# Performance work log

Measured on AMD Instinct MI355X. Metric: run time of the kernel, lower is better.

The kernel has to match this reference:

```python
import jax, jax.numpy as jnp
import numpy as np

S, B, C = 7, 2, 80
LAMBDA_COORDS = 5.0
LAMBDA_NOOBJ = 0.5


def _iou_cxcywh(a, b):
    """Elementwise IoU of boxes in cx,cy,w,h format, shapes (..., 4) -> (...).
    Same math as torchvision box_convert(cxcywh->xyxy) + box_iou diagonal,
    computed directly (O(S^2)) instead of the O(S^4) pairwise matrix."""
    ax1 = a[..., 0] - a[..., 2] * 0.5
    ay1 = a[..., 1] - a[..., 3] * 0.5
    ax2 = a[..., 0] + a[..., 2] * 0.5
    ay2 = a[..., 1] + a[..., 3] * 0.5
    bx1 = b[..., 0] - b[..., 2] * 0.5
    by1 = b[..., 1] - b[..., 3] * 0.5
    bx2 = b[..., 0] + b[..., 2] * 0.5
    by2 = b[..., 1] + b[..., 3] * 0.5
    inter_w = jnp.clip(jnp.minimum(ax2, bx2) - jnp.maximum(ax1, bx1), 0.0)
    inter_h = jnp.clip(jnp.minimum(ay2, by2) - jnp.maximum(ay1, by1), 0.0)
    inter = inter_w * inter_h
    area_a = (ax2 - ax1) * (ay2 - ay1)
    area_b = (bx2 - bx1) * (by2 - by1)
    return inter / (area_a + area_b - inter)


def setup_inputs() -> dict:
    key = jax.random.key(0)
    k1, k2 = jax.random.split(key)
    N = 8192
    predictions = jax.random.normal(k1, (N, S, S, C + 5 * B), dtype=jnp.float32)
    target = jax.random.uniform(k2, (N, S, S, C + 5), dtype=jnp.float32)
    return {"predictions": predictions, "target": target}


def reference(predictions, target):
    preds = predictions.reshape(-1, S, S, C + 5 * B)
    target_boxes = target[..., -4:]                 # (N,S,S,4)
    pred_boxes_1 = preds[..., -4:]
    pred_boxes_2 = preds[..., -9:-5]

    iou1 = _iou_cxcywh(pred_boxes_1, target_boxes)  # (N,S,S) == diag of box_iou
    iou2 = _iou_cxcywh(pred_boxes_2, target_boxes)
    ious_idx = jnp.argmax(jnp.stack([iou1, iou2], axis=0), axis=0)  # (N,S,S)

    m1 = (1 - ious_idx).astype(preds.dtype)  # responsible-box masks
    m2 = ious_idx.astype(preds.dtype)
    obj = target[..., -5]                    # objectness (N,S,S)

    pred_boxes = obj[..., None] * (m1[..., None] * pred_boxes_1 + m2[..., None] * pred_boxes_2)

    dims = jnp.sign(pred_boxes[..., -2:]) * jnp.sqrt(jnp.abs(pred_boxes[..., -2:]) + 1e-6)
    target_dims = jnp.sqrt(target_boxes[..., -2:])

    sse = lambda a, b: jnp.sum((a - b) ** 2)  # MSELoss(reduction='sum')

    center_loss = sse(pred_boxes[..., :-3], target_boxes[..., :-3]) * LAMBDA_COORDS
    dimensions_loss = sse(dims, target_dims) * LAMBDA_COORDS
    coords_loss = center_loss + dimensions_loss

    obj_pred = preds[..., -5] * m1 + preds[..., -10] * m2
    obj_loss = sse(obj * obj_pred, obj)
    noobj_loss = sse((1.0 - obj) * obj_pred, obj) * LAMBDA_NOOBJ

    classes_loss = sse(preds[..., :-10] * obj[..., None], target[..., :-5])

    return (coords_loss, obj_loss, noobj_loss, classes_loss)
```

## Files before the change

### kernel.cpp

```cpp
#include <hip/hip_runtime.h>
#include <stdint.h>


#define NPRED 90
#define NTGT  85
#define NCLS  80
#define CHUNK 32
#define TPB   256
#define NBLK  768

#define NT4 (CHUNK * NTGT / 4)
#define NP4 (CHUNK * NPRED / 4)

#define WAITVM6() asm volatile("s_waitcnt vmcnt(6)" ::: "memory")
#define WAITVM0() asm volatile("s_waitcnt vmcnt(0)" ::: "memory")
#define BARRIER() do { __builtin_amdgcn_sched_barrier(0); \
                       __builtin_amdgcn_s_barrier();      \
                       __builtin_amdgcn_sched_barrier(0); } while (0)

__device__ __forceinline__ void load_lds16(const float4* g, float4* l) {
    __builtin_amdgcn_global_load_lds(
        (const __attribute__((address_space(1))) void*)g,
        (__attribute__((address_space(3))) void*)l,
        16, 0, 0);
}

__device__ __forceinline__ float sgnf(float x) {
    return (x > 0.0f) ? 1.0f : ((x < 0.0f) ? -1.0f : 0.0f);
}

__device__ __forceinline__ float iou_vs_target(
    float acx, float acy, float aw, float ah,
    float bx1, float by1, float bx2, float by2, float area_b)
{
    float ax1 = acx - aw * 0.5f, ay1 = acy - ah * 0.5f;
    float ax2 = acx + aw * 0.5f, ay2 = acy + ah * 0.5f;
    float iw = fmaxf(fminf(ax2, bx2) - fmaxf(ax1, bx1), 0.0f);
    float ih = fmaxf(fminf(ay2, by2) - fmaxf(ay1, by1), 0.0f);
    float inter = iw * ih;
    float area_a = (ax2 - ax1) * (ay2 - ay1);
    return inter / (area_a + area_b - inter);
}

__device__ __forceinline__ void pe(float v, int cl, int j, float obj,
                                   const float* __restrict__ tl, float& clsl)
{
    if (j < NCLS) {
        float d = fmaf(v, obj, -tl[cl * NTGT + j]);
        clsl = fmaf(d, d, clsl);
    }
}

__device__ __forceinline__ void proc_quad(float4 v, int q,
    const float* __restrict__ tl, float& clsl)
{
    int f  = 4 * q;
    int cl = f / NPRED;
    int j  = f - cl * NPRED;
    if (j != 88) {
        float obj = tl[cl * NTGT + NCLS];
        pe(v.x, cl, j,     obj, tl, clsl);
        pe(v.y, cl, j + 1, obj, tl, clsl);
        pe(v.z, cl, j + 2, obj, tl, clsl);
        pe(v.w, cl, j + 3, obj, tl, clsl);
    } else {
        float obj2 = tl[(cl + 1) * NTGT + NCLS];
        pe(v.z, cl + 1, 0, obj2, tl, clsl);
        pe(v.w, cl + 1, 1, obj2, tl, clsl);
    }
}

__device__ __forceinline__ void stage_chunk(
    const float4* __restrict__ tg, const float4* __restrict__ pg,
    float4* tb, float4* pb, int wave, int lane)
{
    if (wave < 2) {
        #pragma unroll
        for (int s = 0; s < 6; ++s) {
            int base = (wave + 2 * s) * 64;
            if (base > NT4 - 64) base = NT4 - 64;
            load_lds16(tg + base + lane, tb + base);
        }
    } else {
        #pragma unroll
        for (int s = 0; s < 6; ++s) {
            int base = ((wave - 2) + 2 * s) * 64;
            if (base > NP4 - 64) base = NP4 - 64;
            load_lds16(pg + base + lane, pb + base);
        }
    }
}

__global__ __launch_bounds__(TPB) void yolo_loss_kernel(
    const float* __restrict__ preds, const float* __restrict__ targ,
    float* __restrict__ part, float* __restrict__ out,
    int n_cells, int mode)
{
    __shared__ float4 tbuf[2][NT4];
    __shared__ float4 pbuf[2][NP4];
    __shared__ float red[4][4];

    float coords = 0.0f, objl = 0.0f, noobjl = 0.0f, clsl = 0.0f;

    const int tid  = threadIdx.x;
    const int wave = tid >> 6;
    const int lane = tid & 63;
    const int n_chunks = n_cells / CHUNK;

    const int start = (int)(((long long)blockIdx.x       * n_chunks) / gridDim.x);
    const int end   = (int)(((long long)(blockIdx.x + 1) * n_chunks) / gridDim.x);

    if (start < end) {
        int cur = 0;
        stage_chunk((const float4*)(targ  + (size_t)start * (CHUNK * NTGT)),
                    (const float4*)(preds + (size_t)start * (CHUNK * NPRED)),
                    tbuf[0], pbuf[0], wave, lane);

        for (int ch = start; ch < end; ++ch) {
            if (ch + 1 < end) {
                stage_chunk((const float4*)(targ  + (size_t)(ch + 1) * (CHUNK * NTGT)),
                            (const float4*)(preds + (size_t)(ch + 1) * (CHUNK * NPRED)),
                            tbuf[cur ^ 1], pbuf[cur ^ 1], wave, lane);
                WAITVM6();
            } else {
                WAITVM0();
            }
            BARRIER();

            const float* tl = (const float*)&tbuf[cur][0];
            const float* pl = (const float*)&pbuf[cur][0];

            proc_quad(pbuf[cur][tid],       tid,       tl, clsl);
            proc_quad(pbuf[cur][tid + 256], tid + 256, tl, clsl);
            if (tid < NP4 - 512)
                proc_quad(pbuf[cur][tid + 512], tid + 512, tl, clsl);

            if (tid < CHUNK) {
                const float* pb = pl + tid * NPRED + NCLS;
                const float* tc = tl + tid * NTGT + NCLS;
                float obj = tc[0];
                float tcx = tc[1], tcy = tc[2], tw = tc[3], th = tc[4];
                float bx1 = tcx - tw * 0.5f, by1 = tcy - th * 0.5f;
                float bx2 = tcx + tw * 0.5f, by2 = tcy + th * 0.5f;
                float area_b = (bx2 - bx1) * (by2 - by1);

                float iou1 = iou_vs_target(pb[6], pb[7], pb[8], pb[9],
                                           bx1, by1, bx2, by2, area_b);
                float iou2 = iou_vs_target(pb[1], pb[2], pb[3], pb[4],
                                           bx1, by1, bx2, by2, area_b);
                bool use2 = iou2 > iou1;

                float pcx = obj * (use2 ? pb[1] : pb[6]);
                float pw  = obj * (use2 ? pb[3] : pb[8]);
                float ph  = obj * (use2 ? pb[4] : pb[9]);

                float dc = pcx - tcx;
                float dw = sgnf(pw) * sqrtf(fabsf(pw) + 1e-6f) - sqrtf(tw);
                float dh = sgnf(ph) * sqrtf(fabsf(ph) + 1e-6f) - sqrtf(th);
                coords = fmaf(dc, dc, coords);
                coords = fmaf(dw, dw, coords);
                coords = fmaf(dh, dh, coords);

                float obj_pred = use2 ? pb[0] : pb[5];
                float e1 = fmaf(obj, obj_pred, -obj);
                objl = fmaf(e1, e1, objl);
                float e2 = fmaf(1.0f - obj, obj_pred, -obj);
                noobjl = fmaf(e2, e2, noobjl);
            }

            BARRIER();
            cur ^= 1;
        }
    }

    for (int cell = n_chunks * CHUNK + (int)(blockIdx.x * TPB + tid);
         cell < n_cells; cell += gridDim.x * TPB) {
        const float* p = preds + (size_t)cell * NPRED;
        const float* t = targ  + (size_t)cell * NTGT;
        float obj = t[NCLS];
        float cls = 0.0f;
        for (int k = 0; k < NCLS; ++k) {
            float d = fmaf(p[k], obj, -t[k]);
            cls = fmaf(d, d, cls);
        }
        clsl += cls;
        float tcx = t[81], tcy = t[82], tw = t[83], th = t[84];
        float bx1 = tcx - tw * 0.5f, by1 = tcy - th * 0.5f;
        float bx2 = tcx + tw * 0.5f, by2 = tcy + th * 0.5f;
        float area_b = (bx2 - bx1) * (by2 - by1);
        float iou1 = iou_vs_target(p[86], p[87], p[88], p[89],
                                   bx1, by1, bx2, by2, area_b);
        float iou2 = iou_vs_target(p[81], p[82], p[83], p[84],
                                   bx1, by1, bx2, by2, area_b);
        bool use2 = iou2 > iou1;
        float pcx = obj * (use2 ? p[81] : p[86]);
        float pw  = obj * (use2 ? p[83] : p[88]);
        float ph  = obj * (use2 ? p[84] : p[89]);
        float dc = pcx - tcx;
        float dw = sgnf(pw) * sqrtf(fabsf(pw) + 1e-6f) - sqrtf(tw);
        float dh = sgnf(ph) * sqrtf(fabsf(ph) + 1e-6f) - sqrtf(th);
        coords = fmaf(dc, dc, coords);
        coords = fmaf(dw, dw, coords);
        coords = fmaf(dh, dh, coords);
        float obj_pred = use2 ? p[80] : p[85];
        float e1 = fmaf(obj, obj_pred, -obj);
        objl = fmaf(e1, e1, objl);
        float e2 = fmaf(1.0f - obj, obj_pred, -obj);
        noobjl = fmaf(e2, e2, noobjl);
    }

    #pragma unroll
    for (int off = 32; off > 0; off >>= 1) {
        coords += __shfl_down(coords, off);
        objl   += __shfl_down(objl, off);
        noobjl += __shfl_down(noobjl, off);
        clsl   += __shfl_down(clsl, off);
    }

    __syncthreads();
    if (lane == 0) {
        red[0][wave] = coords;
        red[1][wave] = objl;
        red[2][wave] = noobjl;
        red[3][wave] = clsl;
    }
    __syncthreads();
    if (tid == 0) {
        float c = red[0][0] + red[0][1] + red[0][2] + red[0][3];
        float o = red[1][0] + red[1][1] + red[1][2] + red[1][3];
        float n = red[2][0] + red[2][1] + red[2][2] + red[2][3];
        float k = red[3][0] + red[3][1] + red[3][2] + red[3][3];
        if (mode == 0) {
            int nb = gridDim.x;
            part[0 * nb + blockIdx.x] = c;
            part[1 * nb + blockIdx.x] = o;
            part[2 * nb + blockIdx.x] = n;
            part[3 * nb + blockIdx.x] = k;
        } else {
            atomicAdd(&out[0], 5.0f * c);
            atomicAdd(&out[1], o);
            atomicAdd(&out[2], 0.5f * n);
            atomicAdd(&out[3], k);
        }
    }
}

__global__ __launch_bounds__(256) void yolo_reduce_kernel(
    const float* __restrict__ part, float* __restrict__ out, int nblk)
{
    int w = threadIdx.x >> 6;
    int lane = threadIdx.x & 63;
    float s = 0.0f;
    for (int i = lane; i < nblk; i += 64) s += part[w * nblk + i];
    #pragma unroll
    for (int off = 32; off > 0; off >>= 1) s += __shfl_down(s, off);
    if (lane == 0) {
        float scale = (w == 0) ? 5.0f : (w == 2) ? 0.5f : 1.0f;
        out[w] = s * scale;
    }
}

extern "C" void kernel_launch(void* const* d_in, const int* in_sizes, int n_in,
                              void* d_out, int out_size, void* d_ws, size_t ws_size,
                              hipStream_t stream) {
    const float* preds = (const float*)d_in[0];
    const float* targ  = (const float*)d_in[1];
    float* out = (float*)d_out;

    int n_cells = in_sizes[0] / NPRED;

    bool use_ws = ws_size >= (size_t)(4 * NBLK) * sizeof(float);

    if (use_ws) {
        float* part = (float*)d_ws;
        hipLaunchKernelGGL(yolo_loss_kernel, dim3(NBLK), dim3(TPB), 0, stream,
                           preds, targ, part, out, n_cells, 0);
        hipLaunchKernelGGL(yolo_reduce_kernel, dim3(1), dim3(256), 0, stream,
                           part, out, NBLK);
        if (out_size > 4) {
            hipMemsetAsync(out + 4, 0, (size_t)(out_size - 4) * sizeof(float), stream);
        }
    } else {
        hipMemsetAsync(d_out, 0, (size_t)out_size * sizeof(float), stream);
        hipLaunchKernelGGL(yolo_loss_kernel, dim3(NBLK), dim3(TPB), 0, stream,
                           preds, targ, (float*)nullptr, out, n_cells, 1);
    }
}
```

Baseline: 302.0 us.

## Pipeline loads per wave, predictions in registers, drop block barriers

Each wave now owns its own range of 8-cell chunks and double-buffers only the target rows in LDS, with global_load_lds. The prediction rows are prefetched straight into registers. The box fields are scattered into a small per-wave LDS scratch area so the IoU lanes can read them. This removes the workgroup-wide s_barriers and the LDS staging of predictions, so the four waves no longer stall on each other and run with less synchronisation. The grid is doubled and launch bounds request higher occupancy, which may raise register pressure from the prefetched float4s.

```diff
diff --git a/kernel.cpp b/kernel.cpp
--- a/kernel.cpp
+++ b/kernel.cpp
@@ -5,24 +5,28 @@
 #define NPRED 90
 #define NTGT  85
 #define NCLS  80
-#define CHUNK 32
+#define CHW   8
 #define TPB   256
-#define NBLK  768
-
-#define NT4 (CHUNK * NTGT / 4)
-#define NP4 (CHUNK * NPRED / 4)
-
+#define NBLK  1536
+
+#define NTW4  (CHW * NTGT / 4)
+#define NPW4  (CHW * NPRED / 4)
+
+#define SBAR()    __builtin_amdgcn_sched_barrier(0)
 #define WAITVM6() asm volatile("s_waitcnt vmcnt(6)" ::: "memory")
 #define WAITVM0() asm volatile("s_waitcnt vmcnt(0)" ::: "memory")
-#define BARRIER() do { __builtin_amdgcn_sched_barrier(0); \
-                       __builtin_amdgcn_s_barrier();      \
-                       __builtin_amdgcn_sched_barrier(0); } while (0)
 
 __device__ __forceinline__ void load_lds16(const float4* g, float4* l) {
     __builtin_amdgcn_global_load_lds(
         (const __attribute__((address_space(1))) void*)g,
         (__attribute__((address_space(3))) void*)l,
         16, 0, 0);
+}
+
+__device__ __forceinline__ void stage_targ(const float4* g, float4* l, int lane) {
+    load_lds16(g + 0   + lane, l + 0);
+    load_lds16(g + 64  + lane, l + 64);
+    load_lds16(g + 106 + lane, l + 106);
 }
 
 __device__ __forceinline__ float sgnf(float x) {
@@ -43,101 +47,100 @@
 }
 
 __device__ __forceinline__ void pe(float v, int cl, int j, float obj,
-                                   const float* __restrict__ tl, float& clsl)
+    const float* __restrict__ tl, float* __restrict__ pbx, float& clsl)
 {
     if (j < NCLS) {
         float d = fmaf(v, obj, -tl[cl * NTGT + j]);
         clsl = fmaf(d, d, clsl);
+    } else {
+        pbx[cl * 11 + (j - NCLS)] = v;
     }
 }
 
 __device__ __forceinline__ void proc_quad(float4 v, int q,
-    const float* __restrict__ tl, float& clsl)
+    const float* __restrict__ tl, float* __restrict__ pbx, float& clsl)
 {
     int f  = 4 * q;
     int cl = f / NPRED;
     int j  = f - cl * NPRED;
     if (j != 88) {
         float obj = tl[cl * NTGT + NCLS];
-        pe(v.x, cl, j,     obj, tl, clsl);
-        pe(v.y, cl, j + 1, obj, tl, clsl);
-        pe(v.z, cl, j + 2, obj, tl, clsl);
-        pe(v.w, cl, j + 3, obj, tl, clsl);
+        pe(v.x, cl, j,     obj, tl, pbx, clsl);
+        pe(v.y, cl, j + 1, obj, tl, pbx, clsl);
+        pe(v.z, cl, j + 2, obj, tl, pbx, clsl);
+        pe(v.w, cl, j + 3, obj, tl, pbx, clsl);
     } else {
+        pbx[cl * 11 + 8] = v.x;
+        pbx[cl * 11 + 9] = v.y;
         float obj2 = tl[(cl + 1) * NTGT + NCLS];
-        pe(v.z, cl + 1, 0, obj2, tl, clsl);
-        pe(v.w, cl + 1, 1, obj2, tl, clsl);
-    }
-}
-
-__device__ __forceinline__ void stage_chunk(
-    const float4* __restrict__ tg, const float4* __restrict__ pg,
-    float4* tb, float4* pb, int wave, int lane)
-{
-    if (wave < 2) {
-        #pragma unroll
-        for (int s = 0; s < 6; ++s) {
-            int base = (wave + 2 * s) * 64;
-            if (base > NT4 - 64) base = NT4 - 64;
-            load_lds16(tg + base + lane, tb + base);
-        }
-    } else {
-        #pragma unroll
-        for (int s = 0; s < 6; ++s) {
-            int base = ((wave - 2) + 2 * s) * 64;
-            if (base > NP4 - 64) base = NP4 - 64;
-            load_lds16(pg + base + lane, pb + base);
-        }
-    }
-}
-
-__global__ __launch_bounds__(TPB) void yolo_loss_kernel(
+        pe(v.z, cl + 1, 0, obj2, tl, pbx, clsl);
+        pe(v.w, cl + 1, 1, obj2, tl, pbx, clsl);
+    }
+}
+
+__global__ __launch_bounds__(TPB, 5) void yolo_loss_kernel(
     const float* __restrict__ preds, const float* __restrict__ targ,
     float* __restrict__ part, float* __restrict__ out,
     int n_cells, int mode)
 {
-    __shared__ float4 tbuf[2][NT4];
-    __shared__ float4 pbuf[2][NP4];
-    __shared__ float red[4][4];
+    __shared__ float4 tring[4][2][NTW4];
+    __shared__ float  pbox[4][88];
+    __shared__ float  red[4][4];
 
     float coords = 0.0f, objl = 0.0f, noobjl = 0.0f, clsl = 0.0f;
 
     const int tid  = threadIdx.x;
     const int wave = tid >> 6;
     const int lane = tid & 63;
-    const int n_chunks = n_cells / CHUNK;
-
-    const int start = (int)(((long long)blockIdx.x       * n_chunks) / gridDim.x);
-    const int end   = (int)(((long long)(blockIdx.x + 1) * n_chunks) / gridDim.x);
-
-    if (start < end) {
-        int cur = 0;
-        stage_chunk((const float4*)(targ  + (size_t)start * (CHUNK * NTGT)),
-                    (const float4*)(preds + (size_t)start * (CHUNK * NPRED)),
-                    tbuf[0], pbuf[0], wave, lane);
-
-        for (int ch = start; ch < end; ++ch) {
-            if (ch + 1 < end) {
-                stage_chunk((const float4*)(targ  + (size_t)(ch + 1) * (CHUNK * NTGT)),
-                            (const float4*)(preds + (size_t)(ch + 1) * (CHUNK * NPRED)),
-                            tbuf[cur ^ 1], pbuf[cur ^ 1], wave, lane);
-                WAITVM6();
-            } else {
-                WAITVM0();
+    const int nch  = n_cells / CHW;
+
+    const long long wid = (long long)blockIdx.x * 4 + wave;
+    const long long W   = (long long)gridDim.x * 4;
+    const int s = (int)((wid * nch) / W);
+    const int e = (int)(((wid + 1) * nch) / W);
+
+    float* tl0 = (float*)&tring[wave][0][0];
+    float* tl1 = (float*)&tring[wave][1][0];
+    float* pbx = &pbox[wave][0];
+
+    float4 pc0 = make_float4(0, 0, 0, 0), pc1 = pc0, pc2 = pc0;
+    float4 pn0 = pc0, pn1 = pc0, pn2 = pc0;
+
+    if (s < e) {
+        {
+            const float4* tg = (const float4*)(targ  + (size_t)s * (CHW * NTGT));
+            const float4* pg = (const float4*)(preds + (size_t)s * (CHW * NPRED));
+            stage_targ(tg, (float4*)((s & 1) ? tl1 : tl0), lane);
+            pc0 = pg[lane];
+            pc1 = pg[64 + lane];
+            pc2 = pg[116 + lane];
+        }
+
+        for (int i = s; i < e; ++i) {
+            const bool hn = (i + 1 < e);
+            if (hn) {
+                const float4* tgn = (const float4*)(targ  + (size_t)(i + 1) * (CHW * NTGT));
+                const float4* pgn = (const float4*)(preds + (size_t)(i + 1) * (CHW * NPRED));
+                stage_targ(tgn, (float4*)(((i + 1) & 1) ? tl1 : tl0), lane);
+                pn0 = pgn[lane];
+                pn1 = pgn[64 + lane];
+                pn2 = pgn[116 + lane];
             }
-            BARRIER();
-
-            const float* tl = (const float*)&tbuf[cur][0];
-            const float* pl = (const float*)&pbuf[cur][0];
-
-            proc_quad(pbuf[cur][tid],       tid,       tl, clsl);
-            proc_quad(pbuf[cur][tid + 256], tid + 256, tl, clsl);
-            if (tid < NP4 - 512)
-                proc_quad(pbuf[cur][tid + 512], tid + 512, tl, clsl);
-
-            if (tid < CHUNK) {
-                const float* pb = pl + tid * NPRED + NCLS;
-                const float* tc = tl + tid * NTGT + NCLS;
+            SBAR();
+            if (hn) { WAITVM6(); }
+            else    { WAITVM0(); }
+            SBAR();
+
+            const float* tl = (i & 1) ? tl1 : tl0;
+
+            proc_quad(pc0, lane,      tl, pbx, clsl);
+            proc_quad(pc1, 64 + lane, tl, pbx, clsl);
+            if (lane >= 12)
+                proc_quad(pc2, 116 + lane, tl, pbx, clsl);
+
+            if (lane < CHW) {
+                const float* pb = pbx + lane * 11;
+                const float* tc = tl + lane * NTGT + NCLS;
                 float obj = tc[0];
                 float tcx = tc[1], tcy = tc[2], tw = tc[3], th = tc[4];
                 float bx1 = tcx - tw * 0.5f, by1 = tcy - th * 0.5f;
@@ -168,12 +171,11 @@
                 noobjl = fmaf(e2, e2, noobjl);
             }
 
-            BARRIER();
-            cur ^= 1;
-        }
-    }
-
-    for (int cell = n_chunks * CHUNK + (int)(blockIdx.x * TPB + tid);
+            pc0 = pn0; pc1 = pn1; pc2 = pn2;
+        }
+    }
+
+    for (int cell = nch * CHW + (int)(blockIdx.x * TPB + tid);
          cell < n_cells; cell += gridDim.x * TPB) {
         const float* p = preds + (size_t)cell * NPRED;
         const float* t = targ  + (size_t)cell * NTGT;
```

After: 307.7 us. Within noise of the previous version (+1.9%).
